# Kernel optimization log

Measured on AMD Instinct MI355X. Metric: run time of the kernel, lower is better.

## Reference

```python
import jax, jax.numpy as jnp
import numpy as np

INPUT_DIM = 1024
OUTPUT_DIM = 1024
DOWN = INPUT_DIM // 8  # reduction_factor=8
NUM_TOKENS = 2


def setup_inputs() -> dict:
    key = jax.random.key(0)
    k1, k2, k3, k4, k5 = jax.random.split(key, 5)
    B, Sx, Sy = 32, 2048, 512
    x = jax.random.normal(k1, (B, Sx, INPUT_DIM), dtype=jnp.float32)
    y = jax.random.normal(k2, (B, Sy, INPUT_DIM), dtype=jnp.float32)
    # nn.Parameter(torch.rand(...)) -> uniform [0,1)
    latent_tokens = jax.random.uniform(k3, (NUM_TOKENS, INPUT_DIM), dtype=jnp.float32)
    gate = jnp.zeros((1,), dtype=jnp.float32)
    # Conv1d kernel_size=1, no bias == pointwise matmul; kaiming-uniform-ish init
    lim_d = 1.0 / np.sqrt(INPUT_DIM)
    lim_u = 1.0 / np.sqrt(DOWN)
    W_down = jax.random.uniform(k4, (DOWN, INPUT_DIM), dtype=jnp.float32, minval=-lim_d, maxval=lim_d)
    W_up = jax.random.uniform(k5, (OUTPUT_DIM, DOWN), dtype=jnp.float32, minval=-lim_u, maxval=lim_u)
    return {"x": x, "y": y, "latent_tokens": latent_tokens, "gate": gate,
            "W_down": W_down, "W_up": W_up}


def reference(x, y, latent_tokens, gate, W_down, W_up):
    # tokens attend over y:  [B,T,Sy] softmax over Sy
    att_y2t = jax.nn.softmax(jnp.einsum('td,bsd->bts', latent_tokens, y), axis=-1)
    tokens = latent_tokens[None] + jnp.einsum('bts,bsd->btd', att_y2t, y)  # [B,T,D]
    # x attends over tokens: [B,Sx,T] softmax over T
    att_t2x = jax.nn.softmax(jnp.einsum('bsd,btd->bst', x, tokens), axis=-1)
    x_res = jnp.einsum('bst,btd->bsd', att_t2x, tokens)
    x = x + gate * x_res
    # 1x1 conv bottleneck: down -> ReLU -> up (pointwise matmuls)
    z = jax.nn.relu(jnp.einsum('bsd,ed->bse', x, W_down))
    out = jnp.einsum('bse,oe->bso', z, W_up)
    return out
```

## Files before the change

kernel.cpp:

```cpp
#include <hip/hip_runtime.h>
#include <hip/hip_bf16.h>

#define B_N 32
#define SX 2048
#define SY 512
#define DIM 1024
#define NTOK 2
#define DN 128
#define ODIM 1024
#define BM 64
#define BK 64
#define NT 16
#define RING 2

typedef __bf16 bf16;
typedef __bf16 bf16x8 __attribute__((ext_vector_type(8)));
typedef __bf16 bf16x4 __attribute__((ext_vector_type(4)));
typedef float f32x4 __attribute__((ext_vector_type(4)));

typedef __attribute__((address_space(3))) unsigned char lds_u8;
typedef const __attribute__((address_space(1))) unsigned char glb_u8;

__device__ __forceinline__ f32x4 mfma16(bf16x8 a, bf16x8 b, f32x4 c) {
  return __builtin_amdgcn_mfma_f32_16x16x32_bf16(a, b, c, 0, 0, 0);
}
__device__ __forceinline__ void gll16(const void* g, void* l) {
  __builtin_amdgcn_global_load_lds((glb_u8*)g, (lds_u8*)l, 16, 0, 0);
}

__global__ __launch_bounds__(256) void prep_kernel(const float* __restrict__ Wd,
                                                   const float* __restrict__ Wu,
                                                   bf16* __restrict__ wdb,
                                                   bf16* __restrict__ wub) {
  int i = blockIdx.x * 256 + threadIdx.x;
  if (i < DN * DIM) {
    wdb[i] = (bf16)Wd[i];
    wub[i] = (bf16)Wu[i];
  }
}

__global__ __launch_bounds__(256) void tokens_kernel(const float* __restrict__ y,
                                                     const float* __restrict__ lat,
                                                     const float* __restrict__ gate,
                                                     float* __restrict__ tokens) {
  if (gate[0] == 0.0f) return;
  __shared__ float s_lat[NTOK][DIM];
  __shared__ float s_sc[NTOK][SY];
  int b = blockIdx.x;
  int tid = threadIdx.x, wave = tid >> 6, lane = tid & 63;
  const float* yb = y + (size_t)b * SY * DIM;
  for (int i = tid; i < NTOK * DIM; i += 256) ((float*)s_lat)[i] = lat[i];
  __syncthreads();
  for (int s = wave * 128; s < wave * 128 + 128; ++s) {
    const float* yr = yb + (size_t)s * DIM;
    float d0 = 0.f, d1 = 0.f;
#pragma unroll
    for (int i = 0; i < 4; ++i) {
      f32x4 v = *(const f32x4*)(yr + lane * 4 + i * 256);
      f32x4 l0 = *(const f32x4*)(&s_lat[0][lane * 4 + i * 256]);
      f32x4 l1 = *(const f32x4*)(&s_lat[1][lane * 4 + i * 256]);
      d0 += v[0] * l0[0] + v[1] * l0[1] + v[2] * l0[2] + v[3] * l0[3];
      d1 += v[0] * l1[0] + v[1] * l1[1] + v[2] * l1[2] + v[3] * l1[3];
    }
#pragma unroll
    for (int off = 32; off > 0; off >>= 1) {
      d0 += __shfl_xor(d0, off);
      d1 += __shfl_xor(d1, off);
    }
    if (lane == 0) { s_sc[0][s] = d0; s_sc[1][s] = d1; }
  }
  __syncthreads();
  if (wave < 2) {
    float m = -3.4e38f;
    for (int s = lane; s < SY; s += 64) m = fmaxf(m, s_sc[wave][s]);
#pragma unroll
    for (int off = 32; off > 0; off >>= 1) m = fmaxf(m, __shfl_xor(m, off));
    float sum = 0.f;
    for (int s = lane; s < SY; s += 64) {
      float e = expf(s_sc[wave][s] - m);
      s_sc[wave][s] = e;
      sum += e;
    }
#pragma unroll
    for (int off = 32; off > 0; off >>= 1) sum += __shfl_xor(sum, off);
    float inv = 1.f / sum;
    for (int s = lane; s < SY; s += 64) s_sc[wave][s] *= inv;
  }
  __syncthreads();
  float a0[4] = {0.f, 0.f, 0.f, 0.f}, a1[4] = {0.f, 0.f, 0.f, 0.f};
  for (int s = 0; s < SY; ++s) {
    float p0 = s_sc[0][s], p1 = s_sc[1][s];
    const float* yr = yb + (size_t)s * DIM;
#pragma unroll
    for (int i = 0; i < 4; ++i) {
      float v = yr[tid + i * 256];
      a0[i] += p0 * v;
      a1[i] += p1 * v;
    }
  }
  float* tb = tokens + (size_t)b * NTOK * DIM;
#pragma unroll
  for (int i = 0; i < 4; ++i) {
    tb[tid + i * 256] = s_lat[0][tid + i * 256] + a0[i];
    tb[DIM + tid + i * 256] = s_lat[1][tid + i * 256] + a1[i];
  }
}

__global__ __launch_bounds__(256) void xprime_kernel(const float* __restrict__ x,
                                                     const float* __restrict__ gate,
                                                     const float* __restrict__ tokens,
                                                     float* __restrict__ xp) {
  float g = gate[0];
  if (g == 0.0f) return;
  __shared__ float s_tok[NTOK][DIM];
  __shared__ float s_c[BM][2];
  int tid = threadIdx.x, w = tid >> 6, lane = tid & 63;
  size_t m0 = (size_t)blockIdx.x * BM;
  int b = (int)(m0 / SX);
  const float* xb = x + m0 * DIM;
  const float* tokb = tokens + (size_t)b * NTOK * DIM;
  for (int i = tid; i < NTOK * DIM; i += 256) ((float*)s_tok)[i] = tokb[i];
  __syncthreads();
  for (int i = 0; i < 16; ++i) {
    int r = w * 16 + i;
    const float* xrow = xb + (size_t)r * DIM;
    float d0 = 0.f, d1 = 0.f;
#pragma unroll
    for (int c = 0; c < 4; ++c) {
      f32x4 v = *(const f32x4*)(xrow + lane * 4 + c * 256);
      f32x4 t0 = *(const f32x4*)(&s_tok[0][lane * 4 + c * 256]);
      f32x4 t1 = *(const f32x4*)(&s_tok[1][lane * 4 + c * 256]);
      d0 += v[0] * t0[0] + v[1] * t0[1] + v[2] * t0[2] + v[3] * t0[3];
      d1 += v[0] * t1[0] + v[1] * t1[1] + v[2] * t1[2] + v[3] * t1[3];
    }
#pragma unroll
    for (int off = 32; off > 0; off >>= 1) {
      d0 += __shfl_xor(d0, off);
      d1 += __shfl_xor(d1, off);
    }
    if (lane == 0) {
      float mm = fmaxf(d0, d1);
      float e0 = expf(d0 - mm), e1 = expf(d1 - mm);
      float inv = g / (e0 + e1);
      s_c[r][0] = e0 * inv;
      s_c[r][1] = e1 * inv;
    }
  }
  __syncthreads();
  float* xpb = xp + m0 * DIM;
  for (int r = w * 16; r < w * 16 + 16; ++r) {
    float c0 = s_c[r][0], c1 = s_c[r][1];
#pragma unroll
    for (int c = 0; c < 4; ++c) {
      f32x4 v = *(const f32x4*)(xb + (size_t)r * DIM + lane * 4 + c * 256);
      f32x4 t0 = *(const f32x4*)(&s_tok[0][lane * 4 + c * 256]);
      f32x4 t1 = *(const f32x4*)(&s_tok[1][lane * 4 + c * 256]);
      f32x4 o;
#pragma unroll
      for (int j = 0; j < 4; ++j) o[j] = v[j] + c0 * t0[j] + c1 * t1[j];
      *(f32x4*)(xpb + (size_t)r * DIM + lane * 4 + c * 256) = o;
    }
  }
}

__global__ __launch_bounds__(512, 4) void main_kernel(const float* __restrict__ x,
                                                      const float* __restrict__ gate,
                                                      const float* __restrict__ xp,
                                                      const bf16* __restrict__ wdb,
                                                      const bf16* __restrict__ wub,
                                                      float* __restrict__ out) {
  __shared__ __align__(16) char smem[81920];

  int tid = threadIdx.x, w = tid >> 6, l = tid & 63;
  int lq = l >> 4, lr = l & 15;
  size_t m0 = (size_t)blockIdx.x * BM;
  float g = gate[0];
  const float* xb = ((g != 0.f) ? xp : x) + m0 * DIM;

  const char* xsrc[2];
  const char* wsrc[2];
#pragma unroll
  for (int j = 0; j < 2; ++j) {
    int xr = w * 8 + j * 4 + (l >> 4);
    int xcb = ((l & 15) * 16) ^ ((j * 4 + (l >> 4)) << 5);
    xsrc[j] = (const char*)xb + (size_t)xr * (DIM * 4) + xcb;
    int wr_ = w * 16 + j * 8 + (l >> 3);
    int wcb = ((l & 7) * 16) ^ ((l >> 3) << 4);
    wsrc[j] = (const char*)wdb + (size_t)wr_ * (DIM * 2) + wcb;
  }

  f32x4 acc[4] = {};

  auto STAGE = [&](int t) {
    int b = t & 1;
#pragma unroll
    for (int j = 0; j < 2; ++j)
      gll16(xsrc[j] + (size_t)t * (BK * 4),
            smem + b * 16384 + (w * 8 + j * 4) * 256);
#pragma unroll
    for (int j = 0; j < 2; ++j)
      gll16(wsrc[j] + (size_t)t * (BK * 2),
            smem + 32768 + b * 16384 + (w * 16 + j * 8) * 128);
  };

  auto COMP = [&](int b) {
    const char* xt = smem + b * 16384;
    const char* wt = smem + 32768 + b * 16384;
    __builtin_amdgcn_s_setprio(1);
#pragma unroll
    for (int kc = 0; kc < 2; ++kc) {
      int dn = w * 16 + lr;
      bf16x8 wdf = *(const bf16x8*)(wt + dn * 128 +
                                    ((kc * 64 + lq * 16) ^ ((lr & 7) << 4)));
#pragma unroll
      for (int mt = 0; mt < 4; ++mt) {
        int row = mt * 16 + lr;
        int sz = (row & 7) << 5;
        int kb = kc * 128 + lq * 32;
        f32x4 a0 = *(const f32x4*)(xt + row * 256 + (kb ^ sz));
        f32x4 a1 = *(const f32x4*)(xt + row * 256 + ((kb + 16) ^ sz));
        bf16x8 xf;
#pragma unroll
        for (int jj = 0; jj < 4; ++jj) {
          xf[jj] = (bf16)a0[jj];
          xf[4 + jj] = (bf16)a1[jj];
        }
        acc[mt] = mfma16(wdf, xf, acc[mt]);
      }
    }
    __builtin_amdgcn_s_setprio(0);
  };

  STAGE(0);

#pragma unroll
  for (int t = 0; t < NT; ++t) {
    if (t + 1 < NT) {
      STAGE(t + 1);
      asm volatile("s_waitcnt vmcnt(4)" ::: "memory");
    } else {
      asm volatile("s_waitcnt vmcnt(0)" ::: "memory");
    }
    __builtin_amdgcn_sched_barrier(0);
    __builtin_amdgcn_s_barrier();
    COMP(t & 1);
    __builtin_amdgcn_sched_barrier(0);
    __builtin_amdgcn_s_barrier();
  }

  char* zls = smem + 65536;
#pragma unroll
  for (int mt = 0; mt < 4; ++mt) {
    int xr = mt * 16 + lr;
    int dn = w * 16 + lq * 4;
    bf16x4 pk;
#pragma unroll
    for (int r = 0; r < 4; ++r) pk[r] = (bf16)fmaxf(acc[mt][r], 0.f);
    *(bf16x4*)(zls + xr * (DN * 2) + ((dn * 2) ^ ((xr & 7) << 4))) = pk;
  }
  __syncthreads();

  bf16x8 zF[4][4];
#pragma unroll
  for (int mt = 0; mt < 4; ++mt)
#pragma unroll
    for (int kt = 0; kt < 4; ++kt) {
      int xr = mt * 16 + lr;
      zF[kt][mt] = *(const bf16x8*)(zls + xr * (DN * 2) +
                                    (((kt * 32 + lq * 8) * 2) ^ ((xr & 7) << 4)));
    }

  float* ob = out + m0 * ODIM;
#pragma unroll 2
  for (int oc16 = 0; oc16 < 8; ++oc16) {
    int base = w * 128 + oc16 * 16;
    bf16x8 wu[4];
#pragma unroll
    for (int kt = 0; kt < 4; ++kt)
      wu[kt] = *(const bf16x8*)(wub + (size_t)(base + lr) * DN + kt * 32 + lq * 8);
    f32x4 a2[4] = {};
#pragma unroll
    for (int kt = 0; kt < 4; ++kt)
#pragma unroll
      for (int mt = 0; mt < 4; ++mt)
        a2[mt] = mfma16(wu[kt], zF[kt][mt], a2[mt]);
#pragma unroll
    for (int mt = 0; mt < 4; ++mt)
      *(f32x4*)(ob + (size_t)(mt * 16 + lr) * ODIM + base + lq * 4) = a2[mt];
  }
}

extern "C" void kernel_launch(void* const* d_in, const int* in_sizes, int n_in,
                              void* d_out, int out_size, void* d_ws, size_t ws_size,
                              hipStream_t stream) {
  const float* x = (const float*)d_in[0];
  const float* y = (const float*)d_in[1];
  const float* lat = (const float*)d_in[2];
  const float* gate = (const float*)d_in[3];
  const float* Wd = (const float*)d_in[4];
  const float* Wu = (const float*)d_in[5];
  float* out = (float*)d_out;
  char* ws = (char*)d_ws;

  float* tokens = (float*)ws;
  bf16* wdb = (bf16*)(ws + 262144);
  bf16* wub = (bf16*)(ws + 524288);

  prep_kernel<<<(DN * DIM + 255) / 256, 256, 0, stream>>>(Wd, Wu, wdb, wub);
  tokens_kernel<<<B_N, 256, 0, stream>>>(y, lat, gate, tokens);
  xprime_kernel<<<(B_N * SX) / BM, 256, 0, stream>>>(x, gate, tokens, out);
  main_kernel<<<(B_N * SX) / BM, 512, 0, stream>>>(x, gate, out, wdb, wub, out);
}
```

Before: 155.6 us.

## Keep W_down in registers and stream full-K 16-row x tiles through LDS

Each wave now holds its whole 16-row slice of the bf16 down-projection weights in registers (32 bf16x8 fragments), so W_down is no longer staged through LDS every K step. x is streamed as 16-row by full-1024 fp32 tiles, double-buffered in 128KB of LDS. Each tile's down-projection, ReLU and up-projection finish before the next tile, so the output is written in 16-row chunks. The cost is heavy register use and 136KB of LDS, which limits residency to one block per CU and weakens latency hiding. W_up is also reloaded from global once per 16-row tile instead of once per 64-row block.

```diff
diff --git a/kernel.cpp b/kernel.cpp
--- a/kernel.cpp
+++ b/kernel.cpp
@@ -9,9 +9,8 @@
 #define DN 128
 #define ODIM 1024
 #define BM 64
-#define BK 64
-#define NT 16
-#define RING 2
+#define TROWS 16
+#define NTL 4
 
 typedef __bf16 bf16;
 typedef __bf16 bf16x8 __attribute__((ext_vector_type(8)));
@@ -163,13 +162,13 @@
   }
 }
 
-__global__ __launch_bounds__(512, 4) void main_kernel(const float* __restrict__ x,
-                                                      const float* __restrict__ gate,
-                                                      const float* __restrict__ xp,
-                                                      const bf16* __restrict__ wdb,
-                                                      const bf16* __restrict__ wub,
-                                                      float* __restrict__ out) {
-  __shared__ __align__(16) char smem[81920];
+__global__ __launch_bounds__(512) void main_kernel(const float* __restrict__ x,
+                                                   const float* __restrict__ gate,
+                                                   const float* __restrict__ xp,
+                                                   const bf16* __restrict__ wdb,
+                                                   const bf16* __restrict__ wub,
+                                                   float* __restrict__ out) {
+  __shared__ __align__(16) char smem[139264];
 
   int tid = threadIdx.x, w = tid >> 6, l = tid & 63;
   int lq = l >> 4, lr = l & 15;
@@ -177,116 +176,91 @@
   float g = gate[0];
   const float* xb = ((g != 0.f) ? xp : x) + m0 * DIM;
 
-  const char* xsrc[2];
-  const char* wsrc[2];
-#pragma unroll
-  for (int j = 0; j < 2; ++j) {
-    int xr = w * 8 + j * 4 + (l >> 4);
-    int xcb = ((l & 15) * 16) ^ ((j * 4 + (l >> 4)) << 5);
-    xsrc[j] = (const char*)xb + (size_t)xr * (DIM * 4) + xcb;
-    int wr_ = w * 16 + j * 8 + (l >> 3);
-    int wcb = ((l & 7) * 16) ^ ((l >> 3) << 4);
-    wsrc[j] = (const char*)wdb + (size_t)wr_ * (DIM * 2) + wcb;
-  }
-
-  f32x4 acc[4] = {};
+  bf16x8 wdr[32];
+  {
+    const bf16* wdp = wdb + (size_t)(w * 16 + lr) * DIM + lq * 8;
+#pragma unroll
+    for (int kc = 0; kc < 32; ++kc) wdr[kc] = *(const bf16x8*)(wdp + kc * 32);
+  }
+
+  int r0 = w * 2, r1 = w * 2 + 1;
+  const char* xs0 = (const char*)xb + (size_t)r0 * 4096 + ((l * 16) ^ ((r0 & 7) << 5));
+  const char* xs1 = (const char*)xb + (size_t)r1 * 4096 + ((l * 16) ^ ((r1 & 7) << 5));
 
   auto STAGE = [&](int t) {
-    int b = t & 1;
-#pragma unroll
-    for (int j = 0; j < 2; ++j)
-      gll16(xsrc[j] + (size_t)t * (BK * 4),
-            smem + b * 16384 + (w * 8 + j * 4) * 256);
-#pragma unroll
-    for (int j = 0; j < 2; ++j)
-      gll16(wsrc[j] + (size_t)t * (BK * 2),
-            smem + 32768 + b * 16384 + (w * 16 + j * 8) * 128);
+    char* buf = smem + (t & 1) * 65536;
+    const char* s0 = xs0 + (size_t)t * 65536;
+    const char* s1 = xs1 + (size_t)t * 65536;
+#pragma unroll
+    for (int c = 0; c < 4; ++c) gll16(s0 + c * 1024, buf + r0 * 4096 + c * 1024);
+#pragma unroll
+    for (int c = 0; c < 4; ++c) gll16(s1 + c * 1024, buf + r1 * 4096 + c * 1024);
   };
 
-  auto COMP = [&](int b) {
-    const char* xt = smem + b * 16384;
-    const char* wt = smem + 32768 + b * 16384;
-    __builtin_amdgcn_s_setprio(1);
-#pragma unroll
-    for (int kc = 0; kc < 2; ++kc) {
-      int dn = w * 16 + lr;
-      bf16x8 wdf = *(const bf16x8*)(wt + dn * 128 +
-                                    ((kc * 64 + lq * 16) ^ ((lr & 7) << 4)));
-#pragma unroll
-      for (int mt = 0; mt < 4; ++mt) {
-        int row = mt * 16 + lr;
-        int sz = (row & 7) << 5;
-        int kb = kc * 128 + lq * 32;
-        f32x4 a0 = *(const f32x4*)(xt + row * 256 + (kb ^ sz));
-        f32x4 a1 = *(const f32x4*)(xt + row * 256 + ((kb + 16) ^ sz));
-        bf16x8 xf;
-#pragma unroll
-        for (int jj = 0; jj < 4; ++jj) {
-          xf[jj] = (bf16)a0[jj];
-          xf[4 + jj] = (bf16)a1[jj];
-        }
-        acc[mt] = mfma16(wdf, xf, acc[mt]);
-      }
-    }
-    __builtin_amdgcn_s_setprio(0);
-  };
+  char* zls = smem + 131072;
+  float* ob = out + m0 * ODIM;
 
   STAGE(0);
 
 #pragma unroll
-  for (int t = 0; t < NT; ++t) {
-    if (t + 1 < NT) {
+  for (int t = 0; t < NTL; ++t) {
+    if (t + 1 < NTL) {
       STAGE(t + 1);
-      asm volatile("s_waitcnt vmcnt(4)" ::: "memory");
+      asm volatile("s_waitcnt vmcnt(8)" ::: "memory");
     } else {
       asm volatile("s_waitcnt vmcnt(0)" ::: "memory");
     }
     __builtin_amdgcn_sched_barrier(0);
     __builtin_amdgcn_s_barrier();
-    COMP(t & 1);
+
+    const char* xt = smem + (t & 1) * 65536;
+    f32x4 acc = {};
+    __builtin_amdgcn_s_setprio(1);
+#pragma unroll
+    for (int kc = 0; kc < 32; ++kc) {
+      int sw = (lr & 7) << 5;
+      int kb = kc * 128 + lq * 32;
+      f32x4 a0 = *(const f32x4*)(xt + lr * 4096 + (kb ^ sw));
+      f32x4 a1 = *(const f32x4*)(xt + lr * 4096 + ((kb ^ sw) + 16));
+      bf16x8 xf;
+#pragma unroll
+      for (int j = 0; j < 4; ++j) {
+        xf[j] = (bf16)a0[j];
+        xf[4 + j] = (bf16)a1[j];
+      }
+      acc = mfma16(wdr[kc], xf, acc);
+    }
+    __builtin_amdgcn_s_setprio(0);
+
+    {
+      int dn = w * 16 + lq * 4;
+      bf16x4 pk;
+#pragma unroll
+      for (int r = 0; r < 4; ++r) pk[r] = (bf16)fmaxf(acc[r], 0.f);
+      *(bf16x4*)(zls + lr * (DN * 2) + ((dn * 2) ^ ((lr & 7) << 4))) = pk;
+    }
+    asm volatile("s_waitcnt lgkmcnt(0)" ::: "memory");
     __builtin_amdgcn_sched_barrier(0);
     __builtin_amdgcn_s_barrier();
-  }
-
-  char* zls = smem + 65536;
-#pragma unroll
-  for (int mt = 0; mt < 4; ++mt) {
-    int xr = mt * 16 + lr;
-    int dn = w * 16 + lq * 4;
-    bf16x4 pk;
-#pragma unroll
-    for (int r = 0; r < 4; ++r) pk[r] = (bf16)fmaxf(acc[mt][r], 0.f);
-    *(bf16x4*)(zls + xr * (DN * 2) + ((dn * 2) ^ ((xr & 7) << 4))) = pk;
-  }
-  __syncthreads();
-
-  bf16x8 zF[4][4];
-#pragma unroll
-  for (int mt = 0; mt < 4; ++mt)
-#pragma unroll
-    for (int kt = 0; kt < 4; ++kt) {
-      int xr = mt * 16 + lr;
-      zF[kt][mt] = *(const bf16x8*)(zls + xr * (DN * 2) +
-                                    (((kt * 32 + lq * 8) * 2) ^ ((xr & 7) << 4)));
-    }
-
-  float* ob = out + m0 * ODIM;
-#pragma unroll 2
-  for (int oc16 = 0; oc16 < 8; ++oc16) {
-    int base = w * 128 + oc16 * 16;
-    bf16x8 wu[4];
+
+    bf16x8 zF[4];
 #pragma unroll
     for (int kt = 0; kt < 4; ++kt)
-      wu[kt] = *(const bf16x8*)(wub + (size_t)(base + lr) * DN + kt * 32 + lq * 8);
-    f32x4 a2[4] = {};
-#pragma unroll
-    for (int kt = 0; kt < 4; ++kt)
-#pragma unroll
-      for (int mt = 0; mt < 4; ++mt)
-        a2[mt] = mfma16(wu[kt], zF[kt][mt], a2[mt]);
-#pragma unroll
-    for (int mt = 0; mt < 4; ++mt)
-      *(f32x4*)(ob + (size_t)(mt * 16 + lr) * ODIM + base + lq * 4) = a2[mt];
+      zF[kt] = *(const bf16x8*)(zls + lr * (DN * 2) +
+                                (((kt * 32 + lq * 8) * 2) ^ ((lr & 7) << 4)));
+    float* obt = ob + (size_t)t * TROWS * ODIM;
+#pragma unroll
+    for (int s = 0; s < 8; ++s) {
+      int base = w * 128 + s * 16;
+      bf16x8 wu[4];
+#pragma unroll
+      for (int kt = 0; kt < 4; ++kt)
+        wu[kt] = *(const bf16x8*)(wub + (size_t)(base + lr) * DN + kt * 32 + lq * 8);
+      f32x4 a2 = {};
+#pragma unroll
+      for (int kt = 0; kt < 4; ++kt) a2 = mfma16(wu[kt], zF[kt], a2);
+      *(f32x4*)(obt + (size_t)lr * ODIM + base + lq * 4) = a2;
+    }
   }
 }
 
```

New measurement: 292.4 us. 1.88x slower.
